# Performance work log

Measured on AMD Instinct MI355X. Metric: run time of the kernel, lower is better.

## Reference

```python
import jax, jax.numpy as jnp
import numpy as np
from jax import lax

GRID_SIZE = 5
SPLINE_ORDER = 3
GRID_RANGE = (-1.0, 1.0)
# (cin, cout, kernel, stride, pad) per KAN conv layer
CONVS = [(3, 16, 7, 2, 3), (16, 32, 3, 2, 1), (32, 64, 3, 2, 1)]


def make_grid(in_features):
    # uniform extended knot grid: (in_features, grid_size + 2*order + 1)
    h = (GRID_RANGE[1] - GRID_RANGE[0]) / GRID_SIZE
    g = jnp.arange(-SPLINE_ORDER, GRID_SIZE + SPLINE_ORDER + 1, dtype=jnp.float32) * h + GRID_RANGE[0]
    return jnp.broadcast_to(g, (in_features, g.shape[0]))


def b_splines(x, grid):
    # x: (N, in)  ->  (N, in, grid_size + order) via Cox-de Boor recursion
    x = x[..., None]
    bases = ((x >= grid[:, :-1]) & (x < grid[:, 1:])).astype(x.dtype)
    for k in range(1, SPLINE_ORDER + 1):
        left = (x - grid[:, : -(k + 1)]) / (grid[:, k:-1] - grid[:, : -(k + 1)])
        right = (grid[:, k + 1:] - x) / (grid[:, k + 1:] - grid[:, 1:-k])
        bases = left * bases[..., :-1] + right * bases[..., 1:]
    return bases


def kan_linear(x, grid, base_w, spline_w, spline_scaler):
    # base path: silu(x) @ W_base^T ; spline path: B(x) contracted with scaled spline coeffs
    base = jax.nn.silu(x) @ base_w.T
    bsp = b_splines(x, grid)                      # (N, in, K)
    scaled = spline_w * spline_scaler[..., None]  # (out, in, K)
    spline = jnp.einsum('nik,oik->no', bsp, scaled)
    return base + spline


def max_pool_2x2(x):
    return lax.reduce_window(x, -jnp.inf, lax.max, (1, 1, 2, 2), (1, 1, 2, 2), 'VALID')


def setup_inputs() -> dict:
    key = jax.random.key(0)
    ks = jax.random.split(key, 16)
    inp = {'x': jax.random.uniform(ks[0], (8, 3, 224, 224), dtype=jnp.float32)}
    dims = [(16, 147), (32, 144), (64, 288)]
    i = 1
    for li, (out_f, in_f) in enumerate(dims):
        inp[f'bw{li}'] = jax.random.normal(ks[i], (out_f, in_f), jnp.float32) / np.sqrt(in_f); i += 1
        inp[f'sw{li}'] = jax.random.normal(ks[i], (out_f, in_f, GRID_SIZE + SPLINE_ORDER), jnp.float32) * 0.1; i += 1
        inp[f'sc{li}'] = 1.0 + 0.1 * jax.random.normal(ks[i], (out_f, in_f), jnp.float32); i += 1
    inp['bwc'] = jax.random.normal(ks[i], (200, 64), jnp.float32) / 8.0; i += 1
    inp['swc'] = jax.random.normal(ks[i], (200, 64, GRID_SIZE + SPLINE_ORDER), jnp.float32) * 0.1; i += 1
    inp['scc'] = 1.0 + 0.1 * jax.random.normal(ks[i], (200, 64), jnp.float32)
    return inp


def reference(x, bw0, sw0, sc0, bw1, sw1, sc1, bw2, sw2, sc2, bwc, swc, scc):
    params = [(bw0, sw0, sc0), (bw1, sw1, sc1), (bw2, sw2, sc2)]
    h = x
    for i, (cin, cout, k, s, p) in enumerate(CONVS):
        # unfold: (B, cin*k*k, Ho, Wo) with channel-major patch ordering (matches torch unfold)
        patches = lax.conv_general_dilated_patches(
            h, (k, k), (s, s), [(p, p), (p, p)],
            dimension_numbers=('NCHW', 'OIHW', 'NCHW'))
        B, F_, Ho, Wo = patches.shape
        flat = patches.transpose(0, 2, 3, 1).reshape(-1, F_)  # (B*Ho*Wo, cin*k*k)
        y = kan_linear(flat, make_grid(F_), *params[i])
        h = y.reshape(B, Ho, Wo, cout).transpose(0, 3, 1, 2)
        h = jax.nn.relu(h)
        if i < len(CONVS) - 1:
            h = max_pool_2x2(h)
    h = h.mean(axis=(2, 3))  # adaptive avg pool to 1x1 + flatten -> (B, 64)
    return kan_linear(h, make_grid(h.shape[1]), bwc, swc, scc)
```

## Files before the change

kernel.cpp:

```cpp
#include <hip/hip_runtime.h>

#define DEV __device__ __forceinline__

typedef _Float16 f16x8 __attribute__((ext_vector_type(8)));
typedef float f32x4 __attribute__((ext_vector_type(4)));
typedef unsigned int u32x4 __attribute__((ext_vector_type(4)));

DEV f16x8 kan_feats8(float x) {
    const float sil = x / (1.0f + __expf(-x));
    const float k0 = (float)(-3) * 0.4f - 1.0f;
    const float t = (x - k0) * 2.5f;
    const float mf = floorf(t);
    const int m = (int)mf;
    const float u = t - mf, v = 1.0f - u;
    const float u2 = u * u, u3 = u2 * u;
    const float N0 = v * v * v * (1.0f / 6.0f);
    const float N1 = (3.0f * u3 - 6.0f * u2 + 4.0f) * (1.0f / 6.0f);
    const float N2 = (-3.0f * u3 + 3.0f * u2 + 3.0f * u + 1.0f) * (1.0f / 6.0f);
    const float N3 = u3 * (1.0f / 6.0f);
    f16x8 g;
    g[0] = (_Float16)sil;
#pragma unroll
    for (int jj = 0; jj < 6; ++jj) {
        const int j = jj + 2;
        float val = 0.0f;
        val = (m == j + 3) ? N0 : val;
        val = (m == j + 2) ? N1 : val;
        val = (m == j + 1) ? N2 : val;
        val = (m == j)     ? N3 : val;
        g[1 + jj] = (_Float16)val;
    }
    g[7] = (_Float16)0.0f;
    return g;
}

DEV void kan_feats9(float x, float* f) {
    f[0] = x / (1.0f + __expf(-x));
    const float k0 = (float)(-3) * 0.4f - 1.0f;
    const float t = (x - k0) * 2.5f;
    const float mf = floorf(t);
    const int m = (int)mf;
    const float u = t - mf, v = 1.0f - u;
    const float u2 = u * u, u3 = u2 * u;
    const float N0 = v * v * v * (1.0f / 6.0f);
    const float N1 = (3.0f * u3 - 6.0f * u2 + 4.0f) * (1.0f / 6.0f);
    const float N2 = (-3.0f * u3 + 3.0f * u2 + 3.0f * u + 1.0f) * (1.0f / 6.0f);
    const float N3 = u3 * (1.0f / 6.0f);
#pragma unroll
    for (int j = 0; j < 8; ++j) {
        float val = 0.0f;
        val = (m == j + 3) ? N0 : val;
        val = (m == j + 2) ? N1 : val;
        val = (m == j + 1) ? N2 : val;
        val = (m == j)     ? N3 : val;
        f[1 + j] = val;
    }
}

__device__ constexpr int d_l0(int ii) {
    const int i = ii > 146 ? 146 : ii;
    const int ci = i / 49, rem = i % 49, kh = rem / 7, kw = rem % 7;
    return ((((kw & 1) * 3 + ci) * 13 + kh) * 19 + (kw >> 1)) * 16;
}
__device__ constexpr int d_l1(int i) {
    const int ch = i / 9, rem = i % 9, kh = rem / 3, kw = rem % 3;
    return ((((kw & 1) * 16 + ch) * 9 + kh) * 5 + (kw >> 1)) * 16;
}

template <int OUT_F, int IN_F>
DEV void pack_oct8(int g, const float* bw, const float* sw, const float* sc,
                   _Float16* W2) {
    const int o = g % OUT_F, i = g / OUT_F;
    f16x8 v;
    if (i < IN_F) {
        const int wi = o * IN_F + i;
        const float s = sc[wi];
        v[0] = (_Float16)bw[wi];
#pragma unroll
        for (int t = 1; t <= 6; ++t) v[t] = (_Float16)(sw[wi * 8 + t + 1] * s);
        v[7] = (_Float16)0.0f;
    } else {
#pragma unroll
        for (int t = 0; t < 8; ++t) v[t] = (_Float16)0.0f;
    }
    *(f16x8*)(W2 + g * 8) = v;
}

#define PS0 2368
#define PS1 4608
#define PS2 18432
#define PS3 12800
#define PS4 25088
#define PSUM (PS0 + PS1 + PS2 + PS3 + PS4)

__global__ __launch_bounds__(256) void prep_k(
    const float* __restrict__ bw0, const float* __restrict__ sw0, const float* __restrict__ sc0,
    const float* __restrict__ bw1, const float* __restrict__ sw1, const float* __restrict__ sc1,
    const float* __restrict__ bw2, const float* __restrict__ sw2, const float* __restrict__ sc2,
    const float* __restrict__ bwc, const float* __restrict__ swc, const float* __restrict__ scc,
    _Float16* __restrict__ W2_0, _Float16* __restrict__ W2_1, _Float16* __restrict__ W2_2,
    float* __restrict__ wcT, float* __restrict__ h2) {
    const int e = blockIdx.x * 256 + threadIdx.x;
    if (e < PS0) {
        pack_oct8<16, 147>(e, bw0, sw0, sc0, W2_0);
    } else if (e < PS0 + PS1) {
        pack_oct8<32, 144>(e - PS0, bw1, sw1, sc1, W2_1);
    } else if (e < PS0 + PS1 + PS2) {
        pack_oct8<64, 288>(e - PS0 - PS1, bw2, sw2, sc2, W2_2);
    } else if (e < PS0 + PS1 + PS2 + PS3) {
        const int ee = e - PS0 - PS1 - PS2;
        const int o = ee % 200, i = ee / 200;
        const int wi = o * 64 + i;
        const float s = scc[wi];
        wcT[(i * 9 + 0) * 200 + o] = bwc[wi];
#pragma unroll
        for (int t = 0; t < 8; ++t)
            wcT[(i * 9 + 1 + t) * 200 + o] = swc[wi * 8 + t] * s;
    } else if (e < PSUM) {
        h2[e - PS0 - PS1 - PS2 - PS3] = 0.0f;
    }
}

__global__ __launch_bounds__(256, 6) void conv0_k(
    const float* __restrict__ x, const _Float16* __restrict__ W2,
    float* __restrict__ p0) {
    __shared__ __align__(16) _Float16 feats[1482 * 8];
    __shared__ float pb[4 * 8 * 16];
    const int tid = threadIdx.x;
    const int vt = blockIdx.x;
    const int b = vt / 196;
    const int r0 = vt - b * 196;
    const int bh = r0 / 7, bw = r0 - (r0 / 7) * 7;
    const int ih0 = bh * 8 - 3, iw0 = bw * 32 - 3;
    for (int t = tid; t < 1482; t += 256) {
        const int iwa = t % 38;
        const int rr = t / 38;
        const int ihp = rr % 13, ci = rr / 13;
        const int ih = ih0 + ihp, iw = iw0 + iwa;
        float xv = 0.0f;
        if (ih >= 0 && ih < 224 && iw >= 0 && iw < 224)
            xv = x[((b * 3 + ci) * 224 + ih) * 224 + iw];
        const int slot = (((iwa & 1) * 3 + ci) * 13 + ihp) * 19 + (iwa >> 1);
        *(f16x8*)(feats + slot * 8) = kan_feats8(xv);
    }
    __syncthreads();
    const int lane = tid & 63, mt = tid >> 6;
    const int l15 = lane & 15, q = lane >> 4;
    const bool q1 = q & 1, q2 = q & 2;
    const char* aBase = (const char*)feats + ((2 * mt) * 19 + l15) * 16;
    const f16x8* __restrict__ Wv = (const f16x8*)W2;
    f32x4 acc = {0.f, 0.f, 0.f, 0.f};
#pragma unroll
    for (int s = 0; s < 37; ++s) {
        const int o0 = d_l0(4 * s), o1 = d_l0(4 * s + 1);
        const int o2 = d_l0(4 * s + 2), o3 = d_l0(4 * s + 3);
        const int e01 = q1 ? o1 : o0;
        const int e23 = q1 ? o3 : o2;
        const int aoff = q2 ? e23 : e01;
        const f16x8 a = *(const f16x8*)(aBase + aoff);
        const f16x8 bf = Wv[(s * 4 + q) * 16 + l15];
        acc = __builtin_amdgcn_mfma_f32_16x16x32_f16(a, bf, acc, 0, 0, 0);
    }
    pb[(mt * 8 + 2 * q + 0) * 16 + l15] = fmaxf(fmaxf(acc[0], 0.f), fmaxf(acc[1], 0.f));
    pb[(mt * 8 + 2 * q + 1) * 16 + l15] = fmaxf(fmaxf(acc[2], 0.f), fmaxf(acc[3], 0.f));
    __syncthreads();
    const int pr = tid >> 7, o = (tid >> 3) & 15, wp = tid & 7;
    const float v = fmaxf(pb[((2 * pr) * 8 + wp) * 16 + o],
                          pb[((2 * pr + 1) * 8 + wp) * 16 + o]);
    p0[((b * 16 + o) * 56 + bh * 2 + pr) * 56 + bw * 8 + wp] = v;
}

__global__ __launch_bounds__(256, 5) void conv1_k(
    const float* __restrict__ p0, const _Float16* __restrict__ W2,
    unsigned int* __restrict__ featP1) {
    __shared__ __align__(16) _Float16 feats[1440 * 8];
    __shared__ float abuf[2 * 32 * 16];
    const int tid = threadIdx.x;
    const int vt = blockIdx.x;
    const int b = vt / 49;
    const int r0 = vt - b * 49;
    const int bh = r0 / 7, bw = r0 - (r0 / 7) * 7;
    const int ih0 = bh * 8 - 1, iw0 = bw * 8 - 1;
    for (int t = tid; t < 1296; t += 256) {
        const int iwp = t % 9;
        int r = t / 9;
        const int ihp = r % 9;
        const int ch = r / 9;
        const int ih = ih0 + ihp, iw = iw0 + iwp;
        float xv = 0.0f;
        if (ih >= 0 && ih < 56 && iw >= 0 && iw < 56)
            xv = p0[((b * 16 + ch) * 56 + ih) * 56 + iw];
        const int slot = (((iwp & 1) * 16 + ch) * 9 + ihp) * 5 + (iwp >> 1);
        *(f16x8*)(feats + slot * 8) = kan_feats8(xv);
    }
    __syncthreads();
    const int lane = tid & 63, w = tid >> 6;
    const int kc = w >> 1, ot = w & 1;
    const int l15 = lane & 15, q = lane >> 4;
    const bool q1 = q & 1, q2 = q & 2;
    const int mh = l15 >> 2, mw = l15 & 3;
    const int ocol = ot * 16 + l15;
    const char* aBase = (const char*)feats + ((2 * mh) * 5 + mw) * 16 + kc * 5760;
    const f16x8* __restrict__ Wv = (const f16x8*)W2;
    f32x4 acc = {0.f, 0.f, 0.f, 0.f};
#pragma unroll
    for (int s = 0; s < 18; ++s) {
        const int o0 = d_l1(4 * s), o1 = d_l1(4 * s + 1);
        const int o2 = d_l1(4 * s + 2), o3 = d_l1(4 * s + 3);
        const int e01 = q1 ? o1 : o0;
        const int e23 = q1 ? o3 : o2;
        const int aoff = q2 ? e23 : e01;
        const f16x8 a = *(const f16x8*)(aBase + aoff);
        const f16x8 bf = Wv[(kc * 72 + s * 4 + q) * 32 + ocol];
        acc = __builtin_amdgcn_mfma_f32_16x16x32_f16(a, bf, acc, 0, 0, 0);
    }
#pragma unroll
    for (int reg = 0; reg < 4; ++reg)
        abuf[(kc * 32 + ocol) * 16 + q * 4 + reg] = acc[reg];
    __syncthreads();
    if (tid < 128) {
        const int o = tid >> 2, pp = tid & 3;
        const int hp = pp >> 1, wp = pp & 1;
        float mx = -1e30f;
#pragma unroll
        for (int dh = 0; dh < 2; ++dh)
#pragma unroll
            for (int dw = 0; dw < 2; ++dw) {
                const int m = (2 * hp + dh) * 4 + 2 * wp + dw;
                const float s = abuf[(0 * 32 + o) * 16 + m] + abuf[(1 * 32 + o) * 16 + m];
                mx = fmaxf(mx, fmaxf(s, 0.0f));
            }
        const f16x8 g = kan_feats8(mx);
        const size_t idx = ((b * 32 + o) * 14 + bh * 2 + hp) * 14 + bw * 2 + wp;
        *(u32x4*)(featP1 + idx * 4) = __builtin_bit_cast(u32x4, g);
    }
}

__global__ __launch_bounds__(256, 4) void conv2_k(
    const unsigned int* __restrict__ fm, const _Float16* __restrict__ W2,
    float* __restrict__ h2) {
    __shared__ __align__(16) unsigned int featW[16 * 132];
    const int tid = threadIdx.x;
    const int c = blockIdx.x % 9, rt = blockIdx.x / 9;
    const int lane = tid & 63, ot = tid >> 6;
    const int q = lane >> 4, l15 = lane & 15;
    const int ocol = ot * 16 + l15;
    const u32x4 F0p = __builtin_bit_cast(u32x4, kan_feats8(0.0f));
    const int i_in = tid & 31, rbase = tid >> 5;
    int hi0[2], wi0[2], pixb[2];
    bool rv[2];
#pragma unroll
    for (int t = 0; t < 2; ++t) {
        const int n = rt * 16 + rbase + t * 8;
        const int wo_ = n % 7, ho_ = (n / 7) % 7, b_ = n / 49;
        rv[t] = (n < 392);
        hi0[t] = ho_ * 2 - 1;
        wi0[t] = wo_ * 2 - 1;
        pixb[t] = b_ * 32 * 14 * 14;
    }
    f32x4 acc = {0.f, 0.f, 0.f, 0.f};
    const f16x8* __restrict__ Wv = (const f16x8*)W2;
    {
        const int ii = c * 32 + i_in;
        const int ci = ii / 9, rem = ii - ci * 9;
        const int kh = rem / 3, kw = rem - kh * 3;
#pragma unroll
        for (int t = 0; t < 2; ++t) {
            const int hi = hi0[t] + kh, wi = wi0[t] + kw;
            const bool v = rv[t] && hi >= 0 && hi < 14 && wi >= 0 && wi < 14;
            u32x4 rec = F0p;
            if (v)
                rec = *(const u32x4*)(fm + (size_t)(pixb[t] + (ci * 14 + hi) * 14 + wi) * 4);
            *(u32x4*)(featW + (rbase + t * 8) * 132 + i_in * 4) = rec;
        }
        __syncthreads();
        const char* arow = (const char*)featW + l15 * 528 + q * 16;
#pragma unroll
        for (int s = 0; s < 8; ++s) {
            const f16x8 a = *(const f16x8*)(arow + s * 64);
            const f16x8 bf = Wv[(c * 32 + s * 4 + q) * 64 + ocol];
            acc = __builtin_amdgcn_mfma_f32_16x16x32_f16(a, bf, acc, 0, 0, 0);
        }
    }
#pragma unroll
    for (int reg = 0; reg < 4; ++reg) {
        const int n = rt * 16 + q * 4 + reg;
        if (n < 392) {
            const int wo_ = n % 7, ho_ = (n / 7) % 7, b_ = n / 49;
            atomicAdd(h2 + ((b_ * 64 + ocol) * 7 + ho_) * 7 + wo_, acc[reg]);
        }
    }
}

__global__ __launch_bounds__(256) void head_k(
    const float* __restrict__ h2, const float* __restrict__ wT,
    float* __restrict__ out) {
    __shared__ float feat[576];
    __shared__ float psum[4 * 64];
    const int tid = threadIdx.x;
    const int n = blockIdx.x >> 2, oc = blockIdx.x & 3;
    if (tid < 64) {
        const float* p = h2 + (n * 64 + tid) * 49;
        float s = 0.0f;
        for (int j = 0; j < 49; ++j) s += fmaxf(p[j], 0.0f);
        float f9[9];
        kan_feats9(s / 49.0f, f9);
#pragma unroll
        for (int t = 0; t < 9; ++t) feat[tid * 9 + t] = f9[t];
    }
    __syncthreads();
    const int js = tid >> 6, ol = tid & 63;
    if (ol < 50) {
        const int o = oc * 50 + ol;
        float sum = 0.0f;
        for (int j = js * 144; j < js * 144 + 144; ++j)
            sum += feat[j] * wT[j * 200 + o];
        psum[js * 64 + ol] = sum;
    }
    __syncthreads();
    if (tid < 50)
        out[n * 200 + oc * 50 + tid] =
            psum[tid] + psum[64 + tid] + psum[128 + tid] + psum[192 + tid];
}

extern "C" void kernel_launch(void* const* d_in, const int* in_sizes, int n_in,
                              void* d_out, int out_size, void* d_ws, size_t ws_size,
                              hipStream_t stream) {
    const float* x   = (const float*)d_in[0];
    const float* bw0 = (const float*)d_in[1];
    const float* sw0 = (const float*)d_in[2];
    const float* sc0 = (const float*)d_in[3];
    const float* bw1 = (const float*)d_in[4];
    const float* sw1 = (const float*)d_in[5];
    const float* sc1 = (const float*)d_in[6];
    const float* bw2 = (const float*)d_in[7];
    const float* sw2 = (const float*)d_in[8];
    const float* sc2 = (const float*)d_in[9];
    const float* bwc = (const float*)d_in[10];
    const float* swc = (const float*)d_in[11];
    const float* scc = (const float*)d_in[12];
    float* out = (float*)d_out;

    char* ws = (char*)d_ws;
    size_t off = 0;
    auto alloc = [&](size_t nbytes) {
        char* p = ws + off;
        off += (nbytes + 255) & ~(size_t)255;
        return p;
    };
    _Float16* W2_0 = (_Float16*)alloc(PS0 * 16);
    _Float16* W2_1 = (_Float16*)alloc(PS1 * 16);
    _Float16* W2_2 = (_Float16*)alloc(PS2 * 16);
    float* wcT = (float*)alloc(576 * 200 * 4);
    float* h2  = (float*)alloc(8 * 64 * 49 * 4);
    float* p0  = (float*)alloc((size_t)8 * 16 * 56 * 56 * 4);
    unsigned int* featP1 = (unsigned int*)alloc((size_t)8 * 32 * 14 * 14 * 16);

    prep_k<<<(PSUM + 255) / 256, 256, 0, stream>>>(
        bw0, sw0, sc0, bw1, sw1, sc1, bw2, sw2, sc2, bwc, swc, scc,
        W2_0, W2_1, W2_2, wcT, h2);
    conv0_k<<<1568, 256, 0, stream>>>(x, W2_0, p0);
    conv1_k<<<392, 256, 0, stream>>>(p0, W2_1, featP1);
    conv2_k<<<225, 256, 0, stream>>>(featP1, W2_2, h2);
    head_k<<<32, 256, 0, stream>>>(h2, wcT, out);
}
```

Measured before the change: 122.5 us.

## Fuse head into conv2 via completion counter and split-K partial buffers

conv2 now writes each channel chunk's partial results to its own slice of a buffer, using write-through stores instead of atomics. Each block then bumps a global completion counter, and the first 32 blocks spin until all 225 blocks are done before running the head computation. The head sums the 9 partials, applies relu and the mean, and does the KAN linear layer. This removes one kernel launch and the h2 zeroing in prep, at the cost of a spin-wait that assumes all 225 blocks are co-resident, plus more reads for the partial reduction.

```diff
diff --git a/kernel.cpp b/kernel.cpp
--- a/kernel.cpp
+++ b/kernel.cpp
@@ -5,6 +5,10 @@
 typedef _Float16 f16x8 __attribute__((ext_vector_type(8)));
 typedef float f32x4 __attribute__((ext_vector_type(4)));
 typedef unsigned int u32x4 __attribute__((ext_vector_type(4)));
+
+DEV void st4_wt(float* p, float v) {
+    asm volatile("global_store_dword %0, %1, off sc0 sc1" :: "v"(p), "v"(v) : "memory");
+}
 
 DEV f16x8 kan_feats8(float x) {
     const float sil = x / (1.0f + __expf(-x));
@@ -90,8 +94,7 @@
 #define PS1 4608
 #define PS2 18432
 #define PS3 12800
-#define PS4 25088
-#define PSUM (PS0 + PS1 + PS2 + PS3 + PS4)
+#define PSUM (PS0 + PS1 + PS2 + PS3 + 1)
 
 __global__ __launch_bounds__(256) void prep_k(
     const float* __restrict__ bw0, const float* __restrict__ sw0, const float* __restrict__ sc0,
@@ -99,7 +102,7 @@
     const float* __restrict__ bw2, const float* __restrict__ sw2, const float* __restrict__ sc2,
     const float* __restrict__ bwc, const float* __restrict__ swc, const float* __restrict__ scc,
     _Float16* __restrict__ W2_0, _Float16* __restrict__ W2_1, _Float16* __restrict__ W2_2,
-    float* __restrict__ wcT, float* __restrict__ h2) {
+    float* __restrict__ wcT, unsigned int* __restrict__ done) {
     const int e = blockIdx.x * 256 + threadIdx.x;
     if (e < PS0) {
         pack_oct8<16, 147>(e, bw0, sw0, sc0, W2_0);
@@ -117,7 +120,7 @@
         for (int t = 0; t < 8; ++t)
             wcT[(i * 9 + 1 + t) * 200 + o] = swc[wi * 8 + t] * s;
     } else if (e < PSUM) {
-        h2[e - PS0 - PS1 - PS2 - PS3] = 0.0f;
+        *done = 0u;
     }
 }
 
@@ -236,12 +239,14 @@
     }
 }
 
-__global__ __launch_bounds__(256, 4) void conv2_k(
+__global__ __launch_bounds__(256, 4) void conv2_head_k(
     const unsigned int* __restrict__ fm, const _Float16* __restrict__ W2,
-    float* __restrict__ h2) {
+    float* __restrict__ h2p, const float* __restrict__ wcT,
+    float* __restrict__ out, unsigned int* __restrict__ done) {
     __shared__ __align__(16) unsigned int featW[16 * 132];
     const int tid = threadIdx.x;
-    const int c = blockIdx.x % 9, rt = blockIdx.x / 9;
+    const int bb = blockIdx.x;
+    const int c = bb % 9, rt = bb / 9;
     const int lane = tid & 63, ot = tid >> 6;
     const int q = lane >> 4, l15 = lane & 15;
     const int ocol = ot * 16 + l15;
@@ -285,24 +290,34 @@
 #pragma unroll
     for (int reg = 0; reg < 4; ++reg) {
         const int n = rt * 16 + q * 4 + reg;
-        if (n < 392) {
-            const int wo_ = n % 7, ho_ = (n / 7) % 7, b_ = n / 49;
-            atomicAdd(h2 + ((b_ * 64 + ocol) * 7 + ho_) * 7 + wo_, acc[reg]);
+        if (n < 392)
+            st4_wt(&h2p[(size_t)(c * 392 + n) * 64 + ocol], acc[reg]);
+    }
+    asm volatile("s_waitcnt vmcnt(0)" ::: "memory");
+    __syncthreads();
+    if (tid == 0)
+        __hip_atomic_fetch_add(done, 1u, __ATOMIC_RELAXED, __HIP_MEMORY_SCOPE_AGENT);
+
+    if (bb >= 32) return;
+
+    if (tid == 0) {
+        while (__hip_atomic_load(done, __ATOMIC_RELAXED, __HIP_MEMORY_SCOPE_AGENT) < 225u)
+            __builtin_amdgcn_s_sleep(2);
+    }
+    __syncthreads();
+
+    float* feat = (float*)featW;
+    float* psum = (float*)featW + 576;
+    const int n = bb >> 2, oc = bb & 3;
+    if (tid < 64) {
+        float s = 0.0f;
+        for (int j = 0; j < 49; ++j) {
+            float tot = 0.0f;
+#pragma unroll
+            for (int cc = 0; cc < 9; ++cc)
+                tot += h2p[(size_t)(cc * 392 + n * 49 + j) * 64 + tid];
+            s += fmaxf(tot, 0.0f);
         }
-    }
-}
-
-__global__ __launch_bounds__(256) void head_k(
-    const float* __restrict__ h2, const float* __restrict__ wT,
-    float* __restrict__ out) {
-    __shared__ float feat[576];
-    __shared__ float psum[4 * 64];
-    const int tid = threadIdx.x;
-    const int n = blockIdx.x >> 2, oc = blockIdx.x & 3;
-    if (tid < 64) {
-        const float* p = h2 + (n * 64 + tid) * 49;
-        float s = 0.0f;
-        for (int j = 0; j < 49; ++j) s += fmaxf(p[j], 0.0f);
         float f9[9];
         kan_feats9(s / 49.0f, f9);
 #pragma unroll
@@ -314,7 +329,7 @@
         const int o = oc * 50 + ol;
         float sum = 0.0f;
         for (int j = js * 144; j < js * 144 + 144; ++j)
-            sum += feat[j] * wT[j * 200 + o];
+            sum += feat[j] * wcT[j * 200 + o];
         psum[js * 64 + ol] = sum;
     }
     __syncthreads();
@@ -352,15 +367,15 @@
     _Float16* W2_1 = (_Float16*)alloc(PS1 * 16);
     _Float16* W2_2 = (_Float16*)alloc(PS2 * 16);
     float* wcT = (float*)alloc(576 * 200 * 4);
-    float* h2  = (float*)alloc(8 * 64 * 49 * 4);
+    float* h2p = (float*)alloc((size_t)9 * 392 * 64 * 4);
     float* p0  = (float*)alloc((size_t)8 * 16 * 56 * 56 * 4);
     unsigned int* featP1 = (unsigned int*)alloc((size_t)8 * 32 * 14 * 14 * 16);
+    unsigned int* done = (unsigned int*)alloc(256);
 
     prep_k<<<(PSUM + 255) / 256, 256, 0, stream>>>(
         bw0, sw0, sc0, bw1, sw1, sc1, bw2, sw2, sc2, bwc, swc, scc,
-        W2_0, W2_1, W2_2, wcT, h2);
+        W2_0, W2_1, W2_2, wcT, done);
     conv0_k<<<1568, 256, 0, stream>>>(x, W2_0, p0);
     conv1_k<<<392, 256, 0, stream>>>(p0, W2_1, featP1);
-    conv2_k<<<225, 256, 0, stream>>>(featP1, W2_2, h2);
-    head_k<<<32, 256, 0, stream>>>(h2, wcT, out);
-}
+    conv2_head_k<<<225, 256, 0, stream>>>(featP1, W2_2, h2p, wcT, out, done);
+}
```

Result: slower. 134.8 us (+10.1%).
